# Optimization experiments

Hardware: AMD Instinct MI355X
Metric: run time of the kernel (lower is better)

## Reference

```python
import jax, jax.numpy as jnp
import numpy as np

B, S, D = 2, 4096, 512
H, DK, DV = 8, 64, 64
LN_EPS = 1e-5
ATTN_EPS = 1e-6


def layer_norm(x, g, b):
    mu = jnp.mean(x, axis=-1, keepdims=True)
    var = jnp.var(x, axis=-1, keepdims=True)
    return (x - mu) * jax.lax.rsqrt(var + LN_EPS) * g + b


def setup_inputs() -> dict:
    key = jax.random.key(0)
    ks = jax.random.split(key, 12)
    s = 1.0 / np.sqrt(D)
    inp = {
        "Q": jax.random.normal(ks[0], (B, S, D), jnp.float32),
        "K": jax.random.normal(ks[1], (B, S, D), jnp.float32),
        "V": jax.random.normal(ks[2], (B, S, D), jnp.float32),
        "W_q": jax.random.normal(ks[3], (D, H * DK), jnp.float32) * s,
        "W_k": jax.random.normal(ks[4], (D, H * DK), jnp.float32) * s,
        "W_v": jax.random.normal(ks[5], (D, H * DV), jnp.float32) * s,
        "W_o": jax.random.normal(ks[6], (H * DV, D), jnp.float32) * s,
        "ln1_g": jnp.ones((D,), jnp.float32),
        "ln1_b": jnp.zeros((D,), jnp.float32),
        "ln2_g": jnp.ones((D,), jnp.float32),
        "ln2_b": jnp.zeros((D,), jnp.float32),
        "w1": jax.random.normal(ks[7], (4 * D, D), jnp.float32) * s,  # torch Linear: (out, in)
        "b1": jnp.zeros((4 * D,), jnp.float32),
        "w2": jax.random.normal(ks[8], (D, 4 * D), jnp.float32) * (1.0 / np.sqrt(4 * D)),
        "b2": jnp.zeros((D,), jnp.float32),
    }
    return inp


def reference(Q, K, V, W_q, W_k, W_v, W_o, ln1_g, ln1_b, ln2_g, ln2_b, w1, b1, w2, b2):
    Qn = layer_norm(Q, ln1_g, ln1_b)
    # project and split heads: [B,S,H,dk] -> [B,H,S,dk]
    q = (Qn @ W_q).reshape(B, S, H, DK).transpose(0, 2, 1, 3)
    k = (K @ W_k).reshape(B, S, H, DK).transpose(0, 2, 1, 3)
    v = (V @ W_v).reshape(B, S, H, DV).transpose(0, 2, 1, 3)
    scores = jnp.einsum("bhqd,bhkd->bhqk", q, k) / (np.sqrt(DK) + ATTN_EPS)
    attn = jax.nn.softmax(scores, axis=-1)  # same as max-subtract softmax
    ctx = jnp.einsum("bhqk,bhkd->bhqd", attn, v)
    ctx = ctx.transpose(0, 2, 1, 3).reshape(B, S, H * DV)
    att_out = ctx @ W_o  # dropout = identity (eval)
    X = Q + att_out
    Xn = layer_norm(X, ln2_g, ln2_b)
    h = jax.nn.gelu(Xn @ w1.T + b1, approximate=False)
    ffn = h @ w2.T + b2
    return X + ffn
```

## Files before the change

kernel.cpp:

```cpp
#include <hip/hip_runtime.h>

typedef unsigned short u16;
typedef __attribute__((ext_vector_type(8))) short short8;
typedef __attribute__((ext_vector_type(4))) float f32x4;
typedef __attribute__((ext_vector_type(16))) float f32x16;
typedef __attribute__((ext_vector_type(4))) unsigned u32x4;

struct __align__(8) us4 { u16 x, y, z, w; };
struct __align__(8) ui2 { unsigned x, y; };

#define CEXP (1.44269504089f / (8.0f + 1e-6f))

__device__ __forceinline__ u16 f2bf(float f) {
  unsigned u = __builtin_bit_cast(unsigned, f);
  unsigned r = (u + 0x7FFFu + ((u >> 16) & 1u)) >> 16;
  return (u16)r;
}

__device__ __forceinline__ unsigned pack_bf2_trunc(float a, float b) {
  return __builtin_amdgcn_perm(__builtin_bit_cast(unsigned, b),
                               __builtin_bit_cast(unsigned, a), 0x07060302u);
}

__device__ __forceinline__ void async_load16(const void* g, void* l) {
  __builtin_amdgcn_global_load_lds((const __attribute__((address_space(1))) void*)g,
                                   (__attribute__((address_space(3))) void*)l, 16, 0, 0);
}

__global__ void prep_weights(const float* __restrict__ Wq, const float* __restrict__ Wk,
                             const float* __restrict__ Wv, const float* __restrict__ Wo,
                             const float* __restrict__ w1, const float* __restrict__ w2,
                             u16* __restrict__ wqkvT, u16* __restrict__ woT,
                             u16* __restrict__ w1b, u16* __restrict__ w2b) {
  const int z = blockIdx.y;
  const int stride = gridDim.x * blockDim.x;
  const int i0 = blockIdx.x * blockDim.x + threadIdx.x;
  if (z < 4) {
    const float* src = z == 0 ? Wq : z == 1 ? Wk : z == 2 ? Wv : Wo;
    u16* dst = z < 3 ? wqkvT + z * 512 * 512 : woT;
    const float scale = (z == 0) ? CEXP : 1.0f;
    for (int i = i0; i < 512 * 512; i += stride) {
      int n = i >> 9, k = i & 511;
      dst[i] = f2bf(src[k * 512 + n] * scale);
    }
  } else {
    const float* src = z == 4 ? w1 : w2;
    u16* dst = z == 4 ? w1b : w2b;
    for (int i = i0; i < 2048 * 512; i += stride) dst[i] = f2bf(src[i]);
  }
}

template <bool KV>
__launch_bounds__(128)
__global__ void ln_cast(const float* __restrict__ X, const float* __restrict__ gw,
                        const float* __restrict__ bw, u16* __restrict__ Y,
                        const float* __restrict__ Kin, const float* __restrict__ Vin,
                        u16* __restrict__ Kb, u16* __restrict__ Vb) {
  const int row = blockIdx.x, t = threadIdx.x;
  const size_t base = (size_t)row * 512;
  float4 x = ((const float4*)(X + base))[t];
  float s = x.x + x.y + x.z + x.w;
  float ss = x.x * x.x + x.y * x.y + x.z * x.z + x.w * x.w;
#pragma unroll
  for (int off = 32; off > 0; off >>= 1) {
    s += __shfl_xor(s, off);
    ss += __shfl_xor(ss, off);
  }
  __shared__ float red[4];
  if ((t & 63) == 0) { red[(t >> 6) * 2] = s; red[(t >> 6) * 2 + 1] = ss; }
  __syncthreads();
  const float tot = red[0] + red[2], tss = red[1] + red[3];
  const float mu = tot * (1.0f / 512.0f);
  const float var = tss * (1.0f / 512.0f) - mu * mu;
  const float rs = rsqrtf(var + 1e-5f);
  float4 g4 = ((const float4*)gw)[t];
  float4 b4 = ((const float4*)bw)[t];
  us4 o;
  o.x = f2bf((x.x - mu) * rs * g4.x + b4.x);
  o.y = f2bf((x.y - mu) * rs * g4.y + b4.y);
  o.z = f2bf((x.z - mu) * rs * g4.z + b4.z);
  o.w = f2bf((x.w - mu) * rs * g4.w + b4.w);
  ((us4*)(Y + base))[t] = o;
  if constexpr (KV) {
    float4 k4 = ((const float4*)(Kin + base))[t];
    float4 v4 = ((const float4*)(Vin + base))[t];
    us4 ko, vo;
    ko.x = f2bf(k4.x); ko.y = f2bf(k4.y); ko.z = f2bf(k4.z); ko.w = f2bf(k4.w);
    vo.x = f2bf(v4.x); vo.y = f2bf(v4.y); vo.z = f2bf(v4.z); vo.w = f2bf(v4.w);
    ((us4*)(Kb + base))[t] = ko;
    ((us4*)(Vb + base))[t] = vo;
  }
}

__launch_bounds__(256, 4)
__global__ void gemm_qkv(const u16* __restrict__ Aq, const u16* __restrict__ Ak,
                         const u16* __restrict__ Av, const u16* __restrict__ Bt,
                         u16* __restrict__ qb, u16* __restrict__ kb, u16* __restrict__ vtb) {
  __shared__ __align__(16) u16 sA[2][128 * 32];
  __shared__ __align__(16) u16 sB[2][128 * 32];
  const int tid = threadIdx.x;
  const int wave = tid >> 6, lane = tid & 63;
  const int l15 = lane & 15, quad = lane >> 4;
  const int qsw = (quad ^ ((l15 >> 1) & 3)) * 8;
  const int m0 = blockIdx.x * 128, n0 = blockIdx.y * 128;
  const int sel = n0 >> 9;
  const u16* A = sel == 0 ? Aq : sel == 1 ? Ak : Av;
  const int wm = (wave >> 1) * 64, wn = (wave & 1) * 64;
  const int u0 = wave * 64 + lane, u1 = u0 + 256;
  const int sw0 = ((u0 & 3) ^ ((u0 >> 3) & 3)) * 8;
  const int K = 512;

  const u16* a0 = A + (size_t)(m0 + (u0 >> 2)) * K + sw0;
  const u16* a1 = A + (size_t)(m0 + (u1 >> 2)) * K + sw0;
  const u16* b0 = Bt + (size_t)(n0 + (u0 >> 2)) * K + sw0;
  const u16* b1p = Bt + (size_t)(n0 + (u1 >> 2)) * K + sw0;

  f32x4 acc[4][4] = {};
  for (int k0 = 0; k0 < K; k0 += 64) {
#pragma unroll
    for (int hf = 0; hf < 2; hf++) {
      const int kk = k0 + hf * 32;
      async_load16(a0 + kk, &sA[hf][wave * 512]);
      async_load16(a1 + kk, &sA[hf][2048 + wave * 512]);
      async_load16(b0 + kk, &sB[hf][wave * 512]);
      async_load16(b1p + kk, &sB[hf][2048 + wave * 512]);
    }
    __syncthreads();
#pragma unroll
    for (int hf = 0; hf < 2; hf++) {
      short8 af[4], bfr[4];
#pragma unroll
      for (int i = 0; i < 4; i++)
        af[i] = *(const short8*)&sA[hf][(wm + i * 16 + l15) * 32 + qsw];
#pragma unroll
      for (int j = 0; j < 4; j++)
        bfr[j] = *(const short8*)&sB[hf][(wn + j * 16 + l15) * 32 + qsw];
#pragma unroll
      for (int i = 0; i < 4; i++)
#pragma unroll
        for (int j = 0; j < 4; j++)
          acc[i][j] = __builtin_amdgcn_mfma_f32_16x16x32_bf16(af[i], bfr[j], acc[i][j], 0, 0, 0);
    }
    __syncthreads();
  }

#pragma unroll
  for (int i = 0; i < 4; i++) {
#pragma unroll
    for (int j = 0; j < 4; j++) {
      const int ocol = ((n0 + wn) & 511) + j * 16 + l15;
      const int row0 = m0 + wm + i * 16 + quad * 4;
      if (sel == 0) {
#pragma unroll
        for (int r = 0; r < 4; r++) qb[(size_t)(row0 + r) * 512 + ocol] = f2bf(acc[i][j][r]);
      } else if (sel == 1) {
        const int d = ocol & 63, hh2 = ocol >> 6;
        const int ks = d >> 4, hik = (d >> 3) & 1, e = d & 7;
#pragma unroll
        for (int r = 0; r < 4; r++) {
          const int row = row0 + r;
          const int bb = row >> 12, keys = row & 4095;
          const size_t addr =
              (((size_t)((bb * 8 + hh2) * 128 + (keys >> 5)) * 4 + ks) * 64 +
               (keys & 31) + 32 * hik) * 8 + e;
          kb[addr] = f2bf(acc[i][j][r]);
        }
      } else {
        const int b = row0 >> 12, s0 = row0 & 4095;
        const int hh = ocol >> 6, cc = ocol & 63;
        us4 pk;
        pk.x = f2bf(acc[i][j][0]); pk.y = f2bf(acc[i][j][1]);
        pk.z = f2bf(acc[i][j][2]); pk.w = f2bf(acc[i][j][3]);
        *(us4*)&vtb[((size_t)((b * 8 + hh) * 64 + cc) << 12) + s0] = pk;
      }
    }
  }
}

template <int EP, int TN, int LB>
__launch_bounds__(256, LB)
__global__ void gemm_bt(const u16* __restrict__ A, const u16* __restrict__ Bt,
                        int M, int N, int K, void* __restrict__ Cp,
                        const float* __restrict__ bias, const float* __restrict__ res) {
  constexpr int MI = (TN == 128) ? 4 : 2;
  __shared__ __align__(16) u16 sA[2][128 * 32];
  __shared__ __align__(16) u16 sB[2][TN * 32];
  const int tid = threadIdx.x;
  const int wave = tid >> 6, lane = tid & 63;
  const int l15 = lane & 15, quad = lane >> 4;
  const int qsw = (quad ^ ((l15 >> 1) & 3)) * 8;
  const int m0 = blockIdx.x * 128, n0 = blockIdx.y * TN;
  const int wm = (TN == 128) ? (wave >> 1) * 64 : wave * 32;
  const int wn = (TN == 128) ? (wave & 1) * 64 : 0;
  const int u0 = wave * 64 + lane, u1 = u0 + 256;
  const int sw0 = ((u0 & 3) ^ ((u0 >> 3) & 3)) * 8;

  const u16* a0 = A + (size_t)(m0 + (u0 >> 2)) * K + sw0;
  const u16* a1 = A + (size_t)(m0 + (u1 >> 2)) * K + sw0;
  const u16* b0 = Bt + (size_t)(n0 + (u0 >> 2)) * K + sw0;

  f32x4 acc[MI][4] = {};
  for (int k0 = 0; k0 < K; k0 += 64) {
#pragma unroll
    for (int hf = 0; hf < 2; hf++) {
      const int kk = k0 + hf * 32;
      async_load16(a0 + kk, &sA[hf][wave * 512]);
      async_load16(a1 + kk, &sA[hf][2048 + wave * 512]);
      async_load16(b0 + kk, &sB[hf][wave * 512]);
      if constexpr (TN == 128) {
        const u16* b1p = Bt + (size_t)(n0 + (u1 >> 2)) * K + sw0;
        async_load16(b1p + kk, &sB[hf][2048 + wave * 512]);
      }
    }
    __syncthreads();
#pragma unroll
    for (int hf = 0; hf < 2; hf++) {
      short8 af[MI], bfr[4];
#pragma unroll
      for (int i = 0; i < MI; i++)
        af[i] = *(const short8*)&sA[hf][(wm + i * 16 + l15) * 32 + qsw];
#pragma unroll
      for (int j = 0; j < 4; j++)
        bfr[j] = *(const short8*)&sB[hf][(wn + j * 16 + l15) * 32 + qsw];
#pragma unroll
      for (int i = 0; i < MI; i++)
#pragma unroll
        for (int j = 0; j < 4; j++)
          acc[i][j] = __builtin_amdgcn_mfma_f32_16x16x32_bf16(af[i], bfr[j], acc[i][j], 0, 0, 0);
    }
    __syncthreads();
  }

#pragma unroll
  for (int i = 0; i < MI; i++) {
#pragma unroll
    for (int j = 0; j < 4; j++) {
      const int col = n0 + wn + j * 16 + l15;
      const int row0 = m0 + wm + i * 16 + quad * 4;
      if (EP == 2) {
        float* C = (float*)Cp;
#pragma unroll
        for (int r = 0; r < 4; r++) {
          size_t idx = (size_t)(row0 + r) * N + col;
          C[idx] = acc[i][j][r] + res[idx];
        }
      } else if (EP == 3) {
        u16* C = (u16*)Cp;
        const float bv = bias[col];
#pragma unroll
        for (int r = 0; r < 4; r++) {
          float xx = acc[i][j][r] + bv;
          float gl = 0.5f * xx * (1.0f + erff(xx * 0.70710678118f));
          C[(size_t)(row0 + r) * N + col] = f2bf(gl);
        }
      } else {
        float* C = (float*)Cp;
        const float bv = bias[col];
#pragma unroll
        for (int r = 0; r < 4; r++) {
          size_t idx = (size_t)(row0 + r) * N + col;
          C[idx] = acc[i][j][r] + bv + res[idx];
        }
      }
    }
  }
}

__launch_bounds__(512, 2)
__global__ void attn_kernel(const u16* __restrict__ qb, const u16* __restrict__ kfrag,
                            const u16* __restrict__ vtb, u16* __restrict__ ctx) {
  __shared__ __align__(16) u16 smem[16896];
  const int tid = threadIdx.x;
  const int wave = tid >> 6, lane = tid & 63;
  const int l31 = lane & 31, hi = lane >> 5;
  const int qg = wave >> 1, kh = wave & 1;
  const int bh = blockIdx.x, b = bh >> 3, h = bh & 7;
  const int q0 = blockIdx.y * 128;
  const size_t rb = (size_t)b * 4096;
  const int qrow = q0 + qg * 32 + l31;

  short8 qf[4];
#pragma unroll
  for (int ks = 0; ks < 4; ks++)
    qf[ks] = *(const short8*)&qb[(rb + qrow) * 512 + h * 64 + ks * 16 + hi * 8];

  int voff[2][2];
#pragma unroll
  for (int vb = 0; vb < 2; vb++) {
    const int vrow = vb * 32 + l31;
    voff[vb][0] = vrow * 64 + (((kh * 4 + hi) ^ (vrow & 7))) * 8;
    voff[vb][1] = vrow * 64 + (((kh * 4 + 2 + hi) ^ (vrow & 7))) * 8;
  }

  const int srow = tid >> 3, ssl = (tid & 7) ^ (srow & 7);
  const u16* vp = vtb + (size_t)(bh * 64 + srow) * 4096 + ssl * 8;
  const int sdst = tid * 8;

  const u16* kp = kfrag + ((size_t)(bh * 128 + kh) * 4) * 512 + lane * 8;

  short8 kc[4];
  f32x16 stA, stB;
  f32x16 ov[2] = {};
  float l_part = 0.f;

  async_load16(vp, &smem[sdst]);
  vp += 64;
  asm volatile("" ::: "memory");
#pragma unroll
  for (int ks = 0; ks < 4; ks++) kc[ks] = *(const short8*)(kp + ks * 512);
  kp += 4096;
  asm volatile("s_waitcnt vmcnt(0)" ::: "memory");
  __builtin_amdgcn_s_barrier();
  stA = (f32x16){};
  __builtin_amdgcn_s_setprio(1);
#pragma unroll
  for (int ks = 0; ks < 4; ks++)
    stA = __builtin_amdgcn_mfma_f32_32x32x16_bf16(kc[ks], qf[ks], stA, 0, 0, 0);
  __builtin_amdgcn_s_setprio(0);
#pragma unroll
  for (int ks = 0; ks < 4; ks++) kc[ks] = *(const short8*)(kp + ks * 512);
  kp += 4096;

#define STEP(T, VB, CUR, NXT)                                                       \
  {                                                                                 \
    if ((T) < 63) {                                                                 \
      async_load16(vp, &smem[(1 - (VB)) * 4096 + sdst]);                            \
      vp += 64;                                                                     \
      asm volatile("" ::: "memory");                                                \
    }                                                                               \
    float p[16];                                                                    \
    _Pragma("unroll") for (int i = 0; i < 16; i++)                                  \
        p[i] = __builtin_amdgcn_exp2f((CUR)[i]);                                    \
    _Pragma("unroll") for (int i = 0; i < 16; i += 4)                               \
        l_part += (p[i] + p[i + 1]) + (p[i + 2] + p[i + 3]);                        \
    if ((T) < 63) {                                                                 \
      (NXT) = (f32x16){};                                                           \
      __builtin_amdgcn_s_setprio(1);                                                \
      _Pragma("unroll") for (int ks = 0; ks < 4; ks++)                              \
        (NXT) = __builtin_amdgcn_mfma_f32_32x32x16_bf16(kc[ks], qf[ks], (NXT), 0, 0, 0); \
      __builtin_amdgcn_s_setprio(0);                                                \
    }                                                                               \
    if ((T) < 62) {                                                                 \
      _Pragma("unroll") for (int ks = 0; ks < 4; ks++)                              \
        kc[ks] = *(const short8*)(kp + ks * 512);                                   \
      kp += 4096;                                                                   \
    }                                                                               \
    unsigned x0 = pack_bf2_trunc(p[0], p[1]), x1 = pack_bf2_trunc(p[2], p[3]);      \
    unsigned x2 = pack_bf2_trunc(p[4], p[5]), x3 = pack_bf2_trunc(p[6], p[7]);      \
    unsigned x4 = pack_bf2_trunc(p[8], p[9]), x5 = pack_bf2_trunc(p[10], p[11]);    \
    unsigned x6 = pack_bf2_trunc(p[12], p[13]), x7 = pack_bf2_trunc(p[14], p[15]);  \
    auto r0 = __builtin_amdgcn_permlane32_swap(x0, x2, false, false);               \
    auto r1 = __builtin_amdgcn_permlane32_swap(x1, x3, false, false);               \
    auto r2 = __builtin_amdgcn_permlane32_swap(x4, x6, false, false);               \
    auto r3 = __builtin_amdgcn_permlane32_swap(x5, x7, false, false);               \
    u32x4 w0 = {r0[0], r1[0], r0[1], r1[1]};                                        \
    u32x4 w1 = {r2[0], r3[0], r2[1], r3[1]};                                        \
    short8 pf0 = __builtin_bit_cast(short8, w0);                                    \
    short8 pf1 = __builtin_bit_cast(short8, w1);                                    \
    __builtin_amdgcn_s_setprio(1);                                                  \
    _Pragma("unroll") for (int vb = 0; vb < 2; vb++) {                              \
      short8 vf0 = *(const short8*)&smem[(VB) * 4096 + voff[vb][0]];                \
      short8 vf1 = *(const short8*)&smem[(VB) * 4096 + voff[vb][1]];                \
      ov[vb] = __builtin_amdgcn_mfma_f32_32x32x16_bf16(vf0, pf0, ov[vb], 0, 0, 0);  \
      ov[vb] = __builtin_amdgcn_mfma_f32_32x32x16_bf16(vf1, pf1, ov[vb], 0, 0, 0);  \
    }                                                                               \
    __builtin_amdgcn_s_setprio(0);                                                  \
    if ((T) < 63) {                                                                 \
      if ((T) < 62)                                                                 \
        asm volatile("s_waitcnt vmcnt(4)" ::: "memory");                            \
      else                                                                          \
        asm volatile("s_waitcnt vmcnt(0)" ::: "memory");                            \
      __builtin_amdgcn_s_barrier();                                                 \
    }                                                                               \
  }

  for (int g = 0; g < 32; g++) {
    STEP(2 * g, 0, stA, stB);
    STEP(2 * g + 1, 1, stB, stA);
  }
#undef STEP

  float l2 = l_part + __shfl_xor(l_part, 32);
  __syncthreads();
  float* mrg = (float*)smem;
  float* mrgl = (float*)smem + 8192;
  if (kh == 1) {
#pragma unroll
    for (int vb = 0; vb < 2; vb++)
#pragma unroll
      for (int e = 0; e < 16; e++)
        mrg[(qg * 32 + vb * 16 + e) * 64 + lane] = ov[vb][e];
    mrgl[qg * 64 + lane] = l2;
  }
  __syncthreads();
  if (kh == 0) {
    const float inv = 1.0f / (l2 + mrgl[qg * 64 + lane]);
#pragma unroll
    for (int vb = 0; vb < 2; vb++) {
#pragma unroll
      for (int rg = 0; rg < 4; rg++) {
        us4 o;
        o.x = f2bf((ov[vb][rg * 4 + 0] + mrg[(qg * 32 + vb * 16 + rg * 4 + 0) * 64 + lane]) * inv);
        o.y = f2bf((ov[vb][rg * 4 + 1] + mrg[(qg * 32 + vb * 16 + rg * 4 + 1) * 64 + lane]) * inv);
        o.z = f2bf((ov[vb][rg * 4 + 2] + mrg[(qg * 32 + vb * 16 + rg * 4 + 2) * 64 + lane]) * inv);
        o.w = f2bf((ov[vb][rg * 4 + 3] + mrg[(qg * 32 + vb * 16 + rg * 4 + 3) * 64 + lane]) * inv);
        *(us4*)&ctx[(rb + qrow) * 512 + h * 64 + vb * 32 + rg * 8 + hi * 4] = o;
      }
    }
  }
}

extern "C" void kernel_launch(void* const* d_in, const int* in_sizes, int n_in,
                              void* d_out, int out_size, void* d_ws, size_t ws_size,
                              hipStream_t stream) {
  (void)in_sizes; (void)n_in; (void)out_size; (void)ws_size;
  const float* Q = (const float*)d_in[0];
  const float* K = (const float*)d_in[1];
  const float* V = (const float*)d_in[2];
  const float* W_q = (const float*)d_in[3];
  const float* W_k = (const float*)d_in[4];
  const float* W_v = (const float*)d_in[5];
  const float* W_o = (const float*)d_in[6];
  const float* ln1_g = (const float*)d_in[7];
  const float* ln1_b = (const float*)d_in[8];
  const float* ln2_g = (const float*)d_in[9];
  const float* ln2_b = (const float*)d_in[10];
  const float* w1 = (const float*)d_in[11];
  const float* b1 = (const float*)d_in[12];
  const float* w2 = (const float*)d_in[13];
  const float* b2 = (const float*)d_in[14];

  char* w = (char*)d_ws;
  const size_t MB = 1u << 20;
  u16* wqkvT = (u16*)(w);
  u16* woT = (u16*)(w + 3 * MB / 2);
  u16* w1b = (u16*)(w + 2 * MB);
  u16* w2b = (u16*)(w + 4 * MB);
  u16* Qn  = (u16*)(w + 6 * MB);
  u16* Kb  = (u16*)(w + 14 * MB);
  u16* Vb  = (u16*)(w + 22 * MB);
  u16* qb  = (u16*)(w + 30 * MB);
  u16* kb  = (u16*)(w + 38 * MB);
  u16* vtb = (u16*)(w + 46 * MB);
  u16* ctx = (u16*)(w + 54 * MB);
  float* X = (float*)(w + 62 * MB);
  u16* Xn  = (u16*)(w + 6 * MB);
  u16* hb  = (u16*)(w + 14 * MB);

  prep_weights<<<dim3(128, 6), 256, 0, stream>>>(W_q, W_k, W_v, W_o, w1, w2,
                                                 wqkvT, woT, w1b, w2b);
  ln_cast<true><<<8192, 128, 0, stream>>>(Q, ln1_g, ln1_b, Qn, K, V, Kb, Vb);
  gemm_qkv<<<dim3(64, 12), 256, 0, stream>>>(Qn, Kb, Vb, wqkvT, qb, kb, vtb);
  attn_kernel<<<dim3(16, 32), 512, 0, stream>>>(qb, kb, vtb, ctx);
  gemm_bt<2, 64, 4><<<dim3(64, 8), 256, 0, stream>>>(ctx, woT, 8192, 512, 512, X, nullptr, Q);
  ln_cast<false><<<8192, 128, 0, stream>>>(X, ln2_g, ln2_b, Xn, nullptr, nullptr, nullptr, nullptr);
  gemm_bt<3, 128, 4><<<dim3(64, 16), 256, 0, stream>>>(Xn, w1b, 8192, 2048, 512, hb, b1, nullptr);
  gemm_bt<4, 64, 4><<<dim3(64, 8), 256, 0, stream>>>(hb, w2b, 8192, 512, 2048, (float*)d_out, b2, X);
}
```

Before: 310.1 us.

## Pre-swizzle V into MFMA fragment layout and load directly to registers

The V projection epilogue now writes V in a per-lane MFMA fragment layout, matching the K fragment layout. The attention kernel then loads V fragments straight from global memory into registers instead of staging V tiles through LDS with async copies and barriers. This removes the shared-memory staging, the LDS reads and the per-step block barriers. The explicit two-stage software pipeline of the QK MFMA is replaced by a simpler loop, so the added global-load latency must be hidden by register prefetch and by occupancy alone.

Result: slower. 324.7 us (+4.7%).

```diff
diff --git a/kernel.cpp b/kernel.cpp
--- a/kernel.cpp
+++ b/kernel.cpp
@@ -166,12 +166,15 @@
           kb[addr] = f2bf(acc[i][j][r]);
         }
       } else {
-        const int b = row0 >> 12, s0 = row0 & 4095;
-        const int hh = ocol >> 6, cc = ocol & 63;
+        const int dv = ocol & 63, hh2 = ocol >> 6;
+        const int bb = row0 >> 12, key = row0 & 4095;
+        const size_t base =
+            (((size_t)((bb * 8 + hh2) * 128 + (key >> 5)) * 4 + ((key >> 4) & 1) * 2 +
+              (dv >> 5)) * 64 + (dv & 31) + 32 * ((key >> 3) & 1)) * 8 + (key & 7);
         us4 pk;
         pk.x = f2bf(acc[i][j][0]); pk.y = f2bf(acc[i][j][1]);
         pk.z = f2bf(acc[i][j][2]); pk.w = f2bf(acc[i][j][3]);
-        *(us4*)&vtb[((size_t)((b * 8 + hh) * 64 + cc) << 12) + s0] = pk;
+        *(us4*)&vtb[base] = pk;
       }
     }
   }
@@ -268,7 +271,7 @@
 
 __launch_bounds__(512, 2)
 __global__ void attn_kernel(const u16* __restrict__ qb, const u16* __restrict__ kfrag,
-                            const u16* __restrict__ vtb, u16* __restrict__ ctx) {
+                            const u16* __restrict__ vfrag, u16* __restrict__ ctx) {
   __shared__ __align__(16) u16 smem[16896];
   const int tid = threadIdx.x;
   const int wave = tid >> 6, lane = tid & 63;
@@ -284,101 +287,62 @@
   for (int ks = 0; ks < 4; ks++)
     qf[ks] = *(const short8*)&qb[(rb + qrow) * 512 + h * 64 + ks * 16 + hi * 8];
 
-  int voff[2][2];
-#pragma unroll
-  for (int vb = 0; vb < 2; vb++) {
-    const int vrow = vb * 32 + l31;
-    voff[vb][0] = vrow * 64 + (((kh * 4 + hi) ^ (vrow & 7))) * 8;
-    voff[vb][1] = vrow * 64 + (((kh * 4 + 2 + hi) ^ (vrow & 7))) * 8;
-  }
-
-  const int srow = tid >> 3, ssl = (tid & 7) ^ (srow & 7);
-  const u16* vp = vtb + (size_t)(bh * 64 + srow) * 4096 + ssl * 8;
-  const int sdst = tid * 8;
-
   const u16* kp = kfrag + ((size_t)(bh * 128 + kh) * 4) * 512 + lane * 8;
-
-  short8 kc[4];
-  f32x16 stA, stB;
+  const u16* vp = vfrag + ((size_t)(bh * 128 + kh) * 4) * 512 + lane * 8;
+
+  short8 kc[4], vc[4];
   f32x16 ov[2] = {};
   float l_part = 0.f;
 
-  async_load16(vp, &smem[sdst]);
-  vp += 64;
-  asm volatile("" ::: "memory");
 #pragma unroll
   for (int ks = 0; ks < 4; ks++) kc[ks] = *(const short8*)(kp + ks * 512);
   kp += 4096;
-  asm volatile("s_waitcnt vmcnt(0)" ::: "memory");
-  __builtin_amdgcn_s_barrier();
-  stA = (f32x16){};
-  __builtin_amdgcn_s_setprio(1);
-#pragma unroll
-  for (int ks = 0; ks < 4; ks++)
-    stA = __builtin_amdgcn_mfma_f32_32x32x16_bf16(kc[ks], qf[ks], stA, 0, 0, 0);
-  __builtin_amdgcn_s_setprio(0);
-#pragma unroll
-  for (int ks = 0; ks < 4; ks++) kc[ks] = *(const short8*)(kp + ks * 512);
-  kp += 4096;
-
-#define STEP(T, VB, CUR, NXT)                                                       \
-  {                                                                                 \
-    if ((T) < 63) {                                                                 \
-      async_load16(vp, &smem[(1 - (VB)) * 4096 + sdst]);                            \
-      vp += 64;                                                                     \
-      asm volatile("" ::: "memory");                                                \
-    }                                                                               \
-    float p[16];                                                                    \
-    _Pragma("unroll") for (int i = 0; i < 16; i++)                                  \
-        p[i] = __builtin_amdgcn_exp2f((CUR)[i]);                                    \
-    _Pragma("unroll") for (int i = 0; i < 16; i += 4)                               \
-        l_part += (p[i] + p[i + 1]) + (p[i + 2] + p[i + 3]);                        \
-    if ((T) < 63) {                                                                 \
-      (NXT) = (f32x16){};                                                           \
-      __builtin_amdgcn_s_setprio(1);                                                \
-      _Pragma("unroll") for (int ks = 0; ks < 4; ks++)                              \
-        (NXT) = __builtin_amdgcn_mfma_f32_32x32x16_bf16(kc[ks], qf[ks], (NXT), 0, 0, 0); \
-      __builtin_amdgcn_s_setprio(0);                                                \
-    }                                                                               \
-    if ((T) < 62) {                                                                 \
-      _Pragma("unroll") for (int ks = 0; ks < 4; ks++)                              \
-        kc[ks] = *(const short8*)(kp + ks * 512);                                   \
-      kp += 4096;                                                                   \
-    }                                                                               \
-    unsigned x0 = pack_bf2_trunc(p[0], p[1]), x1 = pack_bf2_trunc(p[2], p[3]);      \
-    unsigned x2 = pack_bf2_trunc(p[4], p[5]), x3 = pack_bf2_trunc(p[6], p[7]);      \
-    unsigned x4 = pack_bf2_trunc(p[8], p[9]), x5 = pack_bf2_trunc(p[10], p[11]);    \
-    unsigned x6 = pack_bf2_trunc(p[12], p[13]), x7 = pack_bf2_trunc(p[14], p[15]);  \
-    auto r0 = __builtin_amdgcn_permlane32_swap(x0, x2, false, false);               \
-    auto r1 = __builtin_amdgcn_permlane32_swap(x1, x3, false, false);               \
-    auto r2 = __builtin_amdgcn_permlane32_swap(x4, x6, false, false);               \
-    auto r3 = __builtin_amdgcn_permlane32_swap(x5, x7, false, false);               \
-    u32x4 w0 = {r0[0], r1[0], r0[1], r1[1]};                                        \
-    u32x4 w1 = {r2[0], r3[0], r2[1], r3[1]};                                        \
-    short8 pf0 = __builtin_bit_cast(short8, w0);                                    \
-    short8 pf1 = __builtin_bit_cast(short8, w1);                                    \
-    __builtin_amdgcn_s_setprio(1);                                                  \
-    _Pragma("unroll") for (int vb = 0; vb < 2; vb++) {                              \
-      short8 vf0 = *(const short8*)&smem[(VB) * 4096 + voff[vb][0]];                \
-      short8 vf1 = *(const short8*)&smem[(VB) * 4096 + voff[vb][1]];                \
-      ov[vb] = __builtin_amdgcn_mfma_f32_32x32x16_bf16(vf0, pf0, ov[vb], 0, 0, 0);  \
-      ov[vb] = __builtin_amdgcn_mfma_f32_32x32x16_bf16(vf1, pf1, ov[vb], 0, 0, 0);  \
-    }                                                                               \
-    __builtin_amdgcn_s_setprio(0);                                                  \
-    if ((T) < 63) {                                                                 \
-      if ((T) < 62)                                                                 \
-        asm volatile("s_waitcnt vmcnt(4)" ::: "memory");                            \
-      else                                                                          \
-        asm volatile("s_waitcnt vmcnt(0)" ::: "memory");                            \
-      __builtin_amdgcn_s_barrier();                                                 \
-    }                                                                               \
-  }
-
-  for (int g = 0; g < 32; g++) {
-    STEP(2 * g, 0, stA, stB);
-    STEP(2 * g + 1, 1, stB, stA);
-  }
-#undef STEP
+#pragma unroll
+  for (int f = 0; f < 4; f++) vc[f] = *(const short8*)(vp + f * 512);
+  vp += 4096;
+
+  for (int t = 0; t < 64; t++) {
+    f32x16 st = {};
+    __builtin_amdgcn_s_setprio(1);
+#pragma unroll
+    for (int ks = 0; ks < 4; ks++)
+      st = __builtin_amdgcn_mfma_f32_32x32x16_bf16(kc[ks], qf[ks], st, 0, 0, 0);
+    __builtin_amdgcn_s_setprio(0);
+    if (t < 63) {
+#pragma unroll
+      for (int ks = 0; ks < 4; ks++) kc[ks] = *(const short8*)(kp + ks * 512);
+      kp += 4096;
+    }
+    float p[16];
+#pragma unroll
+    for (int i = 0; i < 16; i++) p[i] = __builtin_amdgcn_exp2f(st[i]);
+#pragma unroll
+    for (int i = 0; i < 16; i += 4)
+      l_part += (p[i] + p[i + 1]) + (p[i + 2] + p[i + 3]);
+    unsigned x0 = pack_bf2_trunc(p[0], p[1]), x1 = pack_bf2_trunc(p[2], p[3]);
+    unsigned x2 = pack_bf2_trunc(p[4], p[5]), x3 = pack_bf2_trunc(p[6], p[7]);
+    unsigned x4 = pack_bf2_trunc(p[8], p[9]), x5 = pack_bf2_trunc(p[10], p[11]);
+    unsigned x6 = pack_bf2_trunc(p[12], p[13]), x7 = pack_bf2_trunc(p[14], p[15]);
+    auto r0 = __builtin_amdgcn_permlane32_swap(x0, x2, false, false);
+    auto r1 = __builtin_amdgcn_permlane32_swap(x1, x3, false, false);
+    auto r2 = __builtin_amdgcn_permlane32_swap(x4, x6, false, false);
+    auto r3 = __builtin_amdgcn_permlane32_swap(x5, x7, false, false);
+    u32x4 w0 = {r0[0], r1[0], r0[1], r1[1]};
+    u32x4 w1 = {r2[0], r3[0], r2[1], r3[1]};
+    short8 pf0 = __builtin_bit_cast(short8, w0);
+    short8 pf1 = __builtin_bit_cast(short8, w1);
+    __builtin_amdgcn_s_setprio(1);
+    ov[0] = __builtin_amdgcn_mfma_f32_32x32x16_bf16(vc[0], pf0, ov[0], 0, 0, 0);
+    ov[1] = __builtin_amdgcn_mfma_f32_32x32x16_bf16(vc[1], pf0, ov[1], 0, 0, 0);
+    ov[0] = __builtin_amdgcn_mfma_f32_32x32x16_bf16(vc[2], pf1, ov[0], 0, 0, 0);
+    ov[1] = __builtin_amdgcn_mfma_f32_32x32x16_bf16(vc[3], pf1, ov[1], 0, 0, 0);
+    __builtin_amdgcn_s_setprio(0);
+    if (t < 63) {
+#pragma unroll
+      for (int f = 0; f < 4; f++) vc[f] = *(const short8*)(vp + f * 512);
+      vp += 4096;
+    }
+  }
 
   float l2 = l_part + __shfl_xor(l_part, 32);
   __syncthreads();
```
